# Optimization experiments

Measured on AMD Instinct MI355X. Metric: run time of the kernel, lower is better.

Reference implementation:

```python
import jax, jax.numpy as jnp
import numpy as np

R_CUT = 5.0
N_NODES = 50000
N_EDGES = 400000
N_GRAPHS = 2500
D = 128        # embedding_size (hardcoded by torch.split(..., 128))
N_RBF = 20
N_BLOCKS = 3
PI = 3.141592653589793


def setup_inputs() -> dict:
    key = jax.random.key(0)
    ks = jax.random.split(key, 32)
    w = lambda k, s: (jax.random.normal(k, s) * 0.05).astype(jnp.float32)
    z = jax.random.randint(ks[0], (N_NODES,), 0, 100)
    edges = jax.random.randint(ks[1], (N_EDGES, 2), 0, N_NODES)
    r_ij = jax.random.uniform(ks[2], (N_EDGES, 1), minval=0.8, maxval=R_CUT, dtype=jnp.float32)
    d = jax.random.normal(ks[3], (N_EDGES, 3), dtype=jnp.float32)
    r_ij_normalized = d / jnp.linalg.norm(d, axis=1, keepdims=True)
    graph_idx = jax.random.randint(ks[4], (N_NODES,), 0, N_GRAPHS)
    return {
        "z": z, "edges": edges, "r_ij": r_ij,
        "r_ij_normalized": r_ij_normalized, "graph_idx": graph_idx,
        "emb": w(ks[5], (100, D)),
        # message blocks (stacked over N_BLOCKS)
        "msg_w1": w(ks[6], (N_BLOCKS, D, D)),   "msg_b1": w(ks[7], (N_BLOCKS, D)),
        "msg_w2": w(ks[8], (N_BLOCKS, D, 3 * D)), "msg_b2": w(ks[9], (N_BLOCKS, 3 * D)),
        "rbf_w": w(ks[10], (N_BLOCKS, N_RBF, 3 * D)), "rbf_b": w(ks[11], (N_BLOCKS, 3 * D)),
        # update blocks
        "upd_U": w(ks[12], (N_BLOCKS, D, D)), "upd_V": w(ks[13], (N_BLOCKS, D, D)),
        "upd_w1": w(ks[14], (N_BLOCKS, 2 * D, D)), "upd_b1": w(ks[15], (N_BLOCKS, D)),
        "upd_w2": w(ks[16], (N_BLOCKS, D, 3 * D)), "upd_b2": w(ks[17], (N_BLOCKS, 3 * D)),
        # readout
        "blue_w1": w(ks[18], (D, D)), "blue_b1": w(ks[19], (D,)),
        "blue_w2": w(ks[20], (D, 1)), "blue_b2": w(ks[21], (1,)),
    }


def _rbf(r, r_cut):
    n = jnp.arange(1, N_RBF + 1, dtype=r.dtype)  # [20]
    return jnp.sin(n * PI / r_cut * r) / r        # [E,20]


def _fcut(r, r_cut):
    return jnp.where(r <= r_cut, 0.5 * (jnp.cos(PI * r / r_cut) + 1.0), 0.0)


def painn_forward(z, edges, r_ij, r_ij_normalized, graph_idx, emb,
                  msg_w1, msg_b1, msg_w2, msg_b2, rbf_w, rbf_b,
                  upd_U, upd_V, upd_w1, upd_b1, upd_w2, upd_b2,
                  blue_w1, blue_b1, blue_w2, blue_b2):
    silu = jax.nn.silu
    src = edges[:, 1]  # gathered (neighbor j)
    dst = edges[:, 0]  # scattered (center i)
    s = emb[z]                                           # [N,128]
    v = jnp.zeros((s.shape[0], 3, D), dtype=r_ij.dtype)  # [N,3,128]
    rbf = _rbf(r_ij, R_CUT)                              # [E,20]
    f_c = _fcut(r_ij, R_CUT)                             # [E,1]
    for i in range(N_BLOCKS):
        # --- message block ---
        rbf_fcut = (rbf @ rbf_w[i] + rbf_b[i]) * f_c            # [E,384]
        s_pass = silu(s @ msg_w1[i] + msg_b1[i]) @ msg_w2[i] + msg_b2[i]  # [N,384]
        pass_out = rbf_fcut * s_pass[src]                        # [E,384]
        d_v, d_s, d_rep = jnp.split(pass_out, 3, axis=-1)        # each [E,128]
        delta_v = v[src] * d_v[:, None, :] + r_ij_normalized[:, :, None] * d_rep[:, None, :]
        s = s + jax.ops.segment_sum(d_s, dst, num_segments=N_NODES)
        v = v + jax.ops.segment_sum(delta_v, dst, num_segments=N_NODES)
        # --- update block ---
        U_v = jnp.einsum('nde,ef->ndf', v, upd_U[i])             # [N,3,128]
        V_v = jnp.einsum('nde,ef->ndf', v, upd_V[i])
        V_norm = jnp.linalg.norm(V_v, axis=1)                    # [N,128]
        sv = jnp.concatenate([V_norm, s], axis=1)                # [N,256]
        a = silu(sv @ upd_w1[i] + upd_b1[i]) @ upd_w2[i] + upd_b2[i]  # [N,384]
        avv, asv, ass = jnp.split(a, 3, axis=1)
        s = s + jnp.sum(U_v * V_v, axis=1) * asv + ass
        v = v + avv[:, None, :] * U_v
    blue = silu(s @ blue_w1 + blue_b1) @ blue_w2 + blue_b2       # [N,1]
    return jax.ops.segment_sum(blue, graph_idx, num_segments=N_GRAPHS)  # [G,1]


def reference(z, edges, r_ij, r_ij_normalized, graph_idx, emb,
              msg_w1, msg_b1, msg_w2, msg_b2, rbf_w, rbf_b,
              upd_U, upd_V, upd_w1, upd_b1, upd_w2, upd_b2,
              blue_w1, blue_b1, blue_w2, blue_b2):
    return painn_forward(z, edges, r_ij, r_ij_normalized, graph_idx, emb,
                         msg_w1, msg_b1, msg_w2, msg_b2, rbf_w, rbf_b,
                         upd_U, upd_V, upd_w1, upd_b1, upd_w2, upd_b2,
                         blue_w1, blue_b1, blue_w2, blue_b2)
```

## Files before the change

### kernel.cpp

```cpp
#include <hip/hip_runtime.h>
#include <hip/hip_bf16.h>
#include <math.h>

#define N_NODES 50000
#define N_EDGES 400000
#define N_GRAPHS 2500
#define D 128
#define D3 384
#define N_RBF 20
#define R_CUT 5.0f
#define PI_F 3.14159265358979f
#define NCH 98
#define GEB 16

typedef __attribute__((ext_vector_type(8))) short bf16x8;
typedef __attribute__((ext_vector_type(4))) float f32x4;

__device__ __forceinline__ float silu_f(float x) {
    return x / (1.0f + __expf(-x));
}
__device__ __forceinline__ short f2bf(float x) {
    union { float f; unsigned u; } v; v.f = x;
    unsigned r = (v.u + 0x7FFFu + ((v.u >> 16) & 1u)) >> 16;
    return (short)r;
}
__device__ __forceinline__ float bf2f(short x) {
    union { unsigned u; float f; } v; v.u = ((unsigned)(unsigned short)x) << 16;
    return v.f;
}

#define MAXJOBS 19
struct PackJobs {
    const float* W[MAXJOBS];
    short* P[MAXJOBS];
    int K[MAXJOBS];
    int N[MAXJOBS];
    int boff[MAXJOBS + 1];
    int njobs;
};
__global__ void k_packall(PackJobs jobs) {
    int b = blockIdx.x;
    int j = 0;
    while (j + 1 < jobs.njobs && b >= jobs.boff[j + 1]) ++j;
    int t = (b - jobs.boff[j]) * 256 + threadIdx.x;
    int K = jobs.K[j], N = jobs.N[j];
    int NKT = K / 32;
    int total = (N / 16) * NKT * 64;
    if (t >= total) return;
    const float* W = jobs.W[j];
    short* P = jobs.P[j];
    int lane = t & 63;
    int kt = (t >> 6) % NKT;
    int nt = (t >> 6) / NKT;
    int k0 = kt * 32 + (lane >> 4) * 8;
    int col = nt * 16 + (lane & 15);
    #pragma unroll
    for (int q = 0; q < 8; ++q)
        P[(size_t)t * 8 + q] = f2bf(W[(size_t)(k0 + q) * N + col]);
}

__global__ void k_packrbf(const float* __restrict__ rbf_w, const float* __restrict__ rbf_b,
                          short* __restrict__ P) {
    int t = blockIdx.x * 256 + threadIdx.x;
    if (t >= 3 * 1536) return;
    int i = t / 1536;
    int r = t - i * 1536;
    int lane = r & 63;
    int nt = r >> 6;
    int col = nt * 16 + (lane & 15);
    int k0 = (lane >> 4) * 8;
    const float* W = rbf_w + (size_t)i * N_RBF * D3;
    const float* B = rbf_b + (size_t)i * D3;
    short* out = P + (size_t)i * 12288 + (size_t)r * 8;
    #pragma unroll
    for (int q = 0; q < 8; ++q) {
        int k = k0 + q;
        float v = (k < N_RBF) ? W[(size_t)k * D3 + col] : ((k == N_RBF) ? B[col] : 0.0f);
        out[q] = f2bf(v);
    }
}

template<int K, int N, bool SILU, int AMODE>
__global__ __launch_bounds__(256) void k_gemm(const void* __restrict__ Aptr,
                                              const void* __restrict__ A2ptr,
                                              const short* __restrict__ Bp,
                                              const float* __restrict__ bias,
                                              short* __restrict__ Cbf, int M) {
    constexpr int NKT = K / 32, NNT = N / 16;
    int lane = threadIdx.x & 63, wv = threadIdx.x >> 6;
    int tile = blockIdx.x * 4 + wv;
    if (tile * 16 >= M) return;
    int arow = tile * 16 + (lane & 15);
    int kgrp = (lane >> 4) * 8;

    bf16x8 a[NKT];
    if (AMODE == 0) {
        const short* A = (const short*)Aptr + (size_t)arow * K + kgrp;
        #pragma unroll
        for (int kt = 0; kt < NKT; ++kt) a[kt] = *(const bf16x8*)(A + kt * 32);
    } else if (AMODE == 1) {
        const float* A = (const float*)Aptr + (size_t)arow * K + kgrp;
        #pragma unroll
        for (int kt = 0; kt < NKT; ++kt)
            #pragma unroll
            for (int j = 0; j < 8; ++j) a[kt][j] = f2bf(A[kt * 32 + j]);
    } else {
        const short* A1 = (const short*)Aptr + (size_t)arow * 128 + kgrp;
        const float* A2 = (const float*)A2ptr + (size_t)arow * 128 + kgrp;
        #pragma unroll
        for (int kt = 0; kt < 4 && kt < NKT; ++kt) a[kt] = *(const bf16x8*)(A1 + kt * 32);
        #pragma unroll
        for (int kt = 4; kt < NKT; ++kt)
            #pragma unroll
            for (int j = 0; j < 8; ++j) a[kt][j] = f2bf(A2[(kt - 4) * 32 + j]);
    }

    int crow0 = tile * 16 + (lane >> 4) * 4;
    int ccol = lane & 15;
    const bf16x8* Bv = (const bf16x8*)Bp;
    #pragma unroll
    for (int nt = 0; nt < NNT; ++nt) {
        f32x4 acc = {0.f, 0.f, 0.f, 0.f};
        #pragma unroll
        for (int kt = 0; kt < NKT; ++kt) {
            bf16x8 b = Bv[(nt * NKT + kt) * 64 + lane];
            acc = __builtin_amdgcn_mfma_f32_16x16x32_bf16(a[kt], b, acc, 0, 0, 0);
        }
        int col = nt * 16 + ccol;
        float bs = bias ? bias[col] : 0.0f;
        #pragma unroll
        for (int j = 0; j < 4; ++j) {
            float v = acc[j] + bs;
            if (SILU) v = silu_f(v);
            Cbf[(size_t)(crow0 + j) * N + col] = f2bf(v);
        }
    }
}

__global__ void k_embed(const int* __restrict__ z, const float* __restrict__ emb,
                        float* __restrict__ s) {
    int i = blockIdx.x * blockDim.x + threadIdx.x;
    if (i < N_NODES * D) {
        int n = i >> 7, c = i & 127;
        s[i] = emb[z[n] * D + c];
    }
}

__global__ void k_hist(const int* __restrict__ edges, int* __restrict__ cnt) {
    int e = blockIdx.x * 256 + threadIdx.x;
    if (e < N_EDGES) atomicAdd(&cnt[edges[2 * e]], 1);
}

__global__ void k_scan1(const int* __restrict__ cnt, int* __restrict__ csum) {
    int t = threadIdx.x;
    int g = blockIdx.x * 512 + t;
    int v = (g < N_NODES) ? cnt[g] : 0;
    #pragma unroll
    for (int off = 32; off > 0; off >>= 1) v += __shfl_down(v, off, 64);
    __shared__ int ws[8];
    if ((t & 63) == 0) ws[t >> 6] = v;
    __syncthreads();
    if (t == 0) {
        int sum = 0;
        #pragma unroll
        for (int i = 0; i < 8; ++i) sum += ws[i];
        csum[blockIdx.x] = sum;
    }
}

__global__ void k_scan2(const int* __restrict__ csum, int* __restrict__ cbase) {
    if (threadIdx.x == 0 && blockIdx.x == 0) {
        int s = 0;
        for (int i = 0; i < NCH; ++i) { cbase[i] = s; s += csum[i]; }
    }
}

__global__ void k_scan3(const int* __restrict__ cnt, const int* __restrict__ cbase,
                        int* __restrict__ rowptr) {
    __shared__ int buf[512];
    int t = threadIdx.x;
    int g = blockIdx.x * 512 + t;
    int orig = (g < N_NODES) ? cnt[g] : 0;
    buf[t] = orig;
    __syncthreads();
    for (int off = 1; off < 512; off <<= 1) {
        int v = (t >= off) ? buf[t - off] : 0;
        __syncthreads();
        buf[t] += v;
        __syncthreads();
    }
    if (g < N_NODES) rowptr[g] = cbase[blockIdx.x] + buf[t] - orig;
    if (g == 0 && blockIdx.x == 0) rowptr[N_NODES] = N_EDGES;
}

__global__ void k_scatter(const int* __restrict__ edges, const float* __restrict__ r_ij,
                          const float* __restrict__ rhat, const int* __restrict__ rowptr,
                          int* __restrict__ cursor, int* __restrict__ esrc,
                          short* __restrict__ erbf, float4* __restrict__ erhat) {
    int e = blockIdx.x * 256 + threadIdx.x;
    if (e >= N_EDGES) return;
    int dst = edges[2 * e], src = edges[2 * e + 1];
    int p = rowptr[dst] + atomicAdd(&cursor[dst], 1);
    esrc[p] = src;
    float r = r_ij[e];
    float fc = (r <= R_CUT) ? 0.5f * (cosf(PI_F * r / R_CUT) + 1.0f) : 0.0f;
    float inv_r = 1.0f / r;
    short rec[32];
    #pragma unroll
    for (int k = 0; k < N_RBF; ++k)
        rec[k] = f2bf(sinf((float)(k + 1) * (PI_F / R_CUT) * r) * inv_r * fc);
    rec[20] = f2bf(fc);
    #pragma unroll
    for (int k = 21; k < 32; ++k) rec[k] = 0;
    short* out = erbf + (size_t)p * 32;
    #pragma unroll
    for (int k = 0; k < 32; ++k) out[k] = rec[k];
    float4 rh;
    rh.x = rhat[3 * e]; rh.y = rhat[3 * e + 1]; rh.z = rhat[3 * e + 2]; rh.w = 0.f;
    erhat[p] = rh;
}

__global__ __launch_bounds__(128, 4) void k_edge3(
    const int* __restrict__ rowptr, const int* __restrict__ esrc,
    const short* __restrict__ erbf, const float4* __restrict__ erhat,
    const short* __restrict__ pRbf,
    const short* __restrict__ spass, const short* __restrict__ vold,
    float* __restrict__ s, short* __restrict__ vnew) {
    __shared__ short gate_lds[GEB][D3];
    int tid = threadIdx.x;
    int lane = tid & 63;
    int wv = tid >> 6;
    int c = tid;
    int ntb = wv * 12;
    for (int n = blockIdx.x; n < N_NODES; n += gridDim.x) {
        int p0 = rowptr[n], p1 = rowptr[n + 1];
        float sa = 0.f, va0 = 0.f, va1 = 0.f, va2 = 0.f;
        for (int pb = p0; pb < p1; pb += GEB) {
            int erow = pb + (lane & 15);
            if (erow >= p1) erow = p1 - 1;
            bf16x8 afrag = *(const bf16x8*)(erbf + (size_t)erow * 32 + (lane >> 4) * 8);
            int r0 = (lane >> 4) * 4;
            int fcol = lane & 15;
            #pragma unroll
            for (int t = 0; t < 12; ++t) {
                int nt = ntb + t;
                bf16x8 b = *(const bf16x8*)(pRbf + ((size_t)(nt * 64 + lane)) * 8);
                f32x4 acc = {0.f, 0.f, 0.f, 0.f};
                acc = __builtin_amdgcn_mfma_f32_16x16x32_bf16(afrag, b, acc, 0, 0, 0);
                int col = nt * 16 + fcol;
                #pragma unroll
                for (int j = 0; j < 4; ++j)
                    gate_lds[r0 + j][col] = f2bf(acc[j]);
            }
            __syncthreads();
            int pe = (pb + GEB < p1) ? pb + GEB : p1;
            for (int p = pb; p < pe; ++p) {
                int src = esrc[p];
                float4 rh = erhat[p];
                const short* g = gate_lds[p - pb];
                float a0 = bf2f(g[c]);
                float a1 = bf2f(g[128 + c]);
                float a2 = bf2f(g[256 + c]);
                const short* sp = spass + (size_t)src * D3;
                float dv = a0 * bf2f(sp[c]);
                float ds = a1 * bf2f(sp[128 + c]);
                float dr = a2 * bf2f(sp[256 + c]);
                sa += ds;
                const short* vs = vold + (size_t)src * D3;
                va0 += bf2f(vs[c]) * dv + rh.x * dr;
                va1 += bf2f(vs[128 + c]) * dv + rh.y * dr;
                va2 += bf2f(vs[256 + c]) * dv + rh.z * dr;
            }
            __syncthreads();
        }
        s[(size_t)n * D + c] += sa;
        size_t vb = (size_t)n * D3;
        vnew[vb + c]       = f2bf(bf2f(vold[vb + c]) + va0);
        vnew[vb + 128 + c] = f2bf(bf2f(vold[vb + 128 + c]) + va1);
        vnew[vb + 256 + c] = f2bf(bf2f(vold[vb + 256 + c]) + va2);
    }
}

__global__ void k_svbuild(const short* __restrict__ Vv, short* __restrict__ Vn) {
    int i = blockIdx.x * 256 + threadIdx.x;
    int n = i >> 7, c = i & 127;
    float acc = 0.f;
    #pragma unroll
    for (int d = 0; d < 3; ++d) {
        float v = bf2f(Vv[(size_t)(n * 3 + d) * D + c]);
        acc += v * v;
    }
    Vn[i] = f2bf(sqrtf(acc));
}

__global__ void k_apply(float* __restrict__ s, short* __restrict__ v,
                        const short* __restrict__ Uv, const short* __restrict__ Vv,
                        const short* __restrict__ a_bf) {
    int i = blockIdx.x * 256 + threadIdx.x;
    int n = i >> 7, c = i & 127;
    float avv = bf2f(a_bf[(size_t)n * D3 + c]);
    float asv = bf2f(a_bf[(size_t)n * D3 + 128 + c]);
    float ass = bf2f(a_bf[(size_t)n * D3 + 256 + c]);
    float scal = 0.f;
    float uvr[3];
    #pragma unroll
    for (int d = 0; d < 3; ++d) {
        float u = bf2f(Uv[(size_t)(n * 3 + d) * D + c]);
        float vv = bf2f(Vv[(size_t)(n * 3 + d) * D + c]);
        uvr[d] = u;
        scal += u * vv;
    }
    s[i] += scal * asv + ass;
    #pragma unroll
    for (int d = 0; d < 3; ++d) {
        size_t idx = (size_t)n * D3 + d * 128 + c;
        v[idx] = f2bf(bf2f(v[idx]) + avv * uvr[d]);
    }
}

__global__ void k_blue_dot(const short* __restrict__ h, const int* __restrict__ graph_idx,
                           const float* __restrict__ w2, const float* __restrict__ b2,
                           float* __restrict__ out) {
    __shared__ float red[4];
    int c = threadIdx.x & 127;
    int n = blockIdx.x * 2 + (threadIdx.x >> 7);
    float val = bf2f(h[(size_t)n * D + c]) * w2[c];
    #pragma unroll
    for (int off = 32; off > 0; off >>= 1) val += __shfl_down(val, off, 64);
    if ((threadIdx.x & 63) == 0) red[threadIdx.x >> 6] = val;
    __syncthreads();
    if (threadIdx.x == 0)   atomicAdd(&out[graph_idx[n]], red[0] + red[1] + b2[0]);
    if (threadIdx.x == 128) atomicAdd(&out[graph_idx[n]], red[2] + red[3] + b2[0]);
}

static inline int gemm_grid(int M) { return (M / 16 + 3) / 4; }

extern "C" void kernel_launch(void* const* d_in, const int* in_sizes, int n_in,
                              void* d_out, int out_size, void* d_ws, size_t ws_size,
                              hipStream_t stream) {
    const int*   z         = (const int*)d_in[0];
    const int*   edges     = (const int*)d_in[1];
    const float* r_ij      = (const float*)d_in[2];
    const float* rhat      = (const float*)d_in[3];
    const int*   graph_idx = (const int*)d_in[4];
    const float* emb       = (const float*)d_in[5];
    const float* msg_w1    = (const float*)d_in[6];
    const float* msg_b1    = (const float*)d_in[7];
    const float* msg_w2    = (const float*)d_in[8];
    const float* msg_b2    = (const float*)d_in[9];
    const float* rbf_w     = (const float*)d_in[10];
    const float* rbf_b     = (const float*)d_in[11];
    const float* upd_U     = (const float*)d_in[12];
    const float* upd_V     = (const float*)d_in[13];
    const float* upd_w1    = (const float*)d_in[14];
    const float* upd_b1    = (const float*)d_in[15];
    const float* upd_w2    = (const float*)d_in[16];
    const float* upd_b2    = (const float*)d_in[17];
    const float* blue_w1   = (const float*)d_in[18];
    const float* blue_b1   = (const float*)d_in[19];
    const float* blue_w2   = (const float*)d_in[20];
    const float* blue_b2   = (const float*)d_in[21];
    float* out = (float*)d_out;

    char* ws = (char*)d_ws;
    size_t off = 0;
    auto alloc = [&](size_t bytes) { void* p = ws + off; off += (bytes + 255) & ~(size_t)255; return p; };

    float* s      = (float*)alloc((size_t)N_NODES * D * 4);
    short* bufV0  = (short*)alloc((size_t)N_NODES * D3 * 2);
    short* bufV1  = (short*)alloc((size_t)N_NODES * D3 * 2);
    short* shrd   = (short*)alloc((size_t)N_NODES * D3 * 2);
    short* hbuf   = (short*)alloc((size_t)N_NODES * D * 2);
    short* Vv     = (short*)alloc((size_t)N_NODES * D3 * 2);
    short* Vn     = shrd;
    int*    esrc   = (int*)alloc((size_t)N_EDGES * 4);
    short*  erbf   = (short*)alloc((size_t)N_EDGES * 32 * 2);
    float4* erhat  = (float4*)alloc((size_t)N_EDGES * 16);
    int*    rowptr = (int*)alloc((size_t)(N_NODES + 1) * 4);
    int*    cnt    = (int*)alloc((size_t)N_NODES * 4);
    int*    csum   = (int*)alloc(NCH * 4);
    int*    cbase  = (int*)alloc(NCH * 4);

    short* pBlue = (short*)alloc(16384 * 2);
    short* pRbfAll = (short*)alloc((size_t)3 * 12288 * 2);
    short* pMsgW1[3]; short* pMsgW2[3]; short* pU[3]; short* pV[3]; short* pUpdW1[3]; short* pUpdW2[3];
    for (int i = 0; i < 3; ++i) {
        pMsgW1[i] = (short*)alloc(16384 * 2);
        pMsgW2[i] = (short*)alloc(49152 * 2);
        pU[i]     = (short*)alloc(16384 * 2);
        pV[i]     = (short*)alloc(16384 * 2);
        pUpdW1[i] = (short*)alloc(32768 * 2);
        pUpdW2[i] = (short*)alloc(49152 * 2);
    }

    PackJobs jobs;
    jobs.njobs = 0;
    int bacc = 0;
    auto addjob = [&](const float* W, short* P, int K, int N) {
        int j = jobs.njobs++;
        jobs.W[j] = W; jobs.P[j] = P; jobs.K[j] = K; jobs.N[j] = N;
        jobs.boff[j] = bacc;
        int total = (N / 16) * (K / 32) * 64;
        bacc += (total + 255) / 256;
        jobs.boff[j + 1] = bacc;
    };
    addjob(blue_w1, pBlue, 128, 128);
    for (int i = 0; i < 3; ++i) {
        addjob(msg_w1 + (size_t)i * D * D,     pMsgW1[i], 128, 128);
        addjob(msg_w2 + (size_t)i * D * D3,    pMsgW2[i], 128, 384);
        addjob(upd_U  + (size_t)i * D * D,     pU[i],     128, 128);
        addjob(upd_V  + (size_t)i * D * D,     pV[i],     128, 128);
        addjob(upd_w1 + (size_t)i * 2 * D * D, pUpdW1[i], 256, 128);
        addjob(upd_w2 + (size_t)i * D * D3,    pUpdW2[i], 128, 384);
    }
    k_packall<<<bacc, 256, 0, stream>>>(jobs);
    k_packrbf<<<18, 256, 0, stream>>>(rbf_w, rbf_b, pRbfAll);

    hipMemsetAsync(cnt, 0, (size_t)N_NODES * 4, stream);
    k_hist<<<(N_EDGES + 255) / 256, 256, 0, stream>>>(edges, cnt);
    k_scan1<<<NCH, 512, 0, stream>>>(cnt, csum);
    k_scan2<<<1, 64, 0, stream>>>(csum, cbase);
    k_scan3<<<NCH, 512, 0, stream>>>(cnt, cbase, rowptr);
    hipMemsetAsync(cnt, 0, (size_t)N_NODES * 4, stream);
    k_scatter<<<(N_EDGES + 255) / 256, 256, 0, stream>>>(edges, r_ij, rhat, rowptr, cnt,
                                                         esrc, erbf, erhat);

    hipMemsetAsync(bufV0, 0, (size_t)N_NODES * D3 * 2, stream);
    hipMemsetAsync(d_out, 0, (size_t)out_size * sizeof(float), stream);
    k_embed<<<(N_NODES * D) / 256, 256, 0, stream>>>(z, emb, s);

    const int gN  = gemm_grid(N_NODES);
    const int gN3 = gemm_grid(N_NODES * 3);

    for (int i = 0; i < 3; ++i) {
        short* vstate = (i & 1) ? bufV1 : bufV0;
        short* vscr   = (i & 1) ? bufV0 : bufV1;
        k_gemm<128, 128, true, 1><<<gN, 256, 0, stream>>>(
            s, nullptr, pMsgW1[i], msg_b1 + (size_t)i * D, hbuf, N_NODES);
        k_gemm<128, 384, false, 0><<<gN, 256, 0, stream>>>(
            hbuf, nullptr, pMsgW2[i], msg_b2 + (size_t)i * D3, shrd, N_NODES);
        k_edge3<<<2048, 128, 0, stream>>>(rowptr, esrc, erbf, erhat,
                                          pRbfAll + (size_t)i * 12288,
                                          shrd, vstate, s, vscr);
        k_gemm<128, 128, false, 0><<<gN3, 256, 0, stream>>>(
            vscr, nullptr, pU[i], nullptr, vstate, N_NODES * 3);
        k_gemm<128, 128, false, 0><<<gN3, 256, 0, stream>>>(
            vscr, nullptr, pV[i], nullptr, Vv, N_NODES * 3);
        k_svbuild<<<(N_NODES * D) / 256, 256, 0, stream>>>(Vv, Vn);
        k_gemm<256, 128, true, 2><<<gN, 256, 0, stream>>>(
            Vn, s, pUpdW1[i], upd_b1 + (size_t)i * D, hbuf, N_NODES);
        k_gemm<128, 384, false, 0><<<gN, 256, 0, stream>>>(
            hbuf, nullptr, pUpdW2[i], upd_b2 + (size_t)i * D3, shrd, N_NODES);
        k_apply<<<(N_NODES * D) / 256, 256, 0, stream>>>(s, vscr, vstate, Vv, shrd);
    }

    k_gemm<128, 128, true, 1><<<gN, 256, 0, stream>>>(
        s, nullptr, pBlue, blue_b1, hbuf, N_NODES);
    k_blue_dot<<<N_NODES / 2, 256, 0, stream>>>(hbuf, graph_idx, blue_w2, blue_b2, out);
}
```

Measured before the change: 1.131 ms.

## Fuse U/V gemms and restructure edge kernel LDS usage and grid

Merges the two per-block U and V projections into one kernel that reads the vector state once and writes both outputs, with the packed weights placed contiguously. In the edge kernel, the RBF weight fragments are hoisted into registers outside the node loop. Edge source indices and unit vectors are staged in shared memory, the gate buffer gets a padded stride to reduce bank conflicts, and the grid is doubled. This cuts repeated global loads and one full pass over the vector state, at the cost of more registers per thread in both kernels.

```diff
diff --git a/kernel.cpp b/kernel.cpp
--- a/kernel.cpp
+++ b/kernel.cpp
@@ -12,6 +12,7 @@
 #define PI_F 3.14159265358979f
 #define NCH 98
 #define GEB 16
+#define GLDS_STRIDE 388
 
 typedef __attribute__((ext_vector_type(8))) short bf16x8;
 typedef __attribute__((ext_vector_type(4))) float f32x4;
@@ -137,6 +138,37 @@
     }
 }
 
+__global__ __launch_bounds__(256) void k_gemmUV(const short* __restrict__ A,
+                                                const short* __restrict__ Bp,
+                                                short* __restrict__ Cu,
+                                                short* __restrict__ Cv, int M) {
+    int lane = threadIdx.x & 63, wv = threadIdx.x >> 6;
+    int tile = blockIdx.x * 4 + wv;
+    if (tile * 16 >= M) return;
+    int arow = tile * 16 + (lane & 15);
+    int kgrp = (lane >> 4) * 8;
+    const short* Ar = A + (size_t)arow * 128 + kgrp;
+    bf16x8 a[4];
+    #pragma unroll
+    for (int kt = 0; kt < 4; ++kt) a[kt] = *(const bf16x8*)(Ar + kt * 32);
+    int crow0 = tile * 16 + (lane >> 4) * 4;
+    int ccol = lane & 15;
+    const bf16x8* Bv = (const bf16x8*)Bp;
+    #pragma unroll
+    for (int nt = 0; nt < 16; ++nt) {
+        f32x4 acc = {0.f, 0.f, 0.f, 0.f};
+        #pragma unroll
+        for (int kt = 0; kt < 4; ++kt)
+            acc = __builtin_amdgcn_mfma_f32_16x16x32_bf16(a[kt], Bv[(nt * 4 + kt) * 64 + lane], acc, 0, 0, 0);
+        int col = nt * 16 + ccol;
+        short* C = (col < 128) ? Cu : Cv;
+        int cc = col & 127;
+        #pragma unroll
+        for (int j = 0; j < 4; ++j)
+            C[(size_t)(crow0 + j) * 128 + cc] = f2bf(acc[j]);
+    }
+}
+
 __global__ void k_embed(const int* __restrict__ z, const float* __restrict__ emb,
                         float* __restrict__ s) {
     int i = blockIdx.x * blockDim.x + threadIdx.x;
@@ -226,12 +258,20 @@
     const short* __restrict__ pRbf,
     const short* __restrict__ spass, const short* __restrict__ vold,
     float* __restrict__ s, short* __restrict__ vnew) {
-    __shared__ short gate_lds[GEB][D3];
+    __shared__ short gate_lds[GEB * GLDS_STRIDE];
+    __shared__ int   src_lds[GEB];
+    __shared__ float4 rh_lds[GEB];
     int tid = threadIdx.x;
     int lane = tid & 63;
     int wv = tid >> 6;
     int c = tid;
     int ntb = wv * 12;
+    bf16x8 bfr[12];
+    #pragma unroll
+    for (int t = 0; t < 12; ++t)
+        bfr[t] = *(const bf16x8*)(pRbf + ((size_t)((ntb + t) * 64 + lane)) * 8);
+    int r0 = (lane >> 4) * 4;
+    int fcol = lane & 15;
     for (int n = blockIdx.x; n < N_NODES; n += gridDim.x) {
         int p0 = rowptr[n], p1 = rowptr[n + 1];
         float sa = 0.f, va0 = 0.f, va1 = 0.f, va2 = 0.f;
@@ -239,25 +279,25 @@
             int erow = pb + (lane & 15);
             if (erow >= p1) erow = p1 - 1;
             bf16x8 afrag = *(const bf16x8*)(erbf + (size_t)erow * 32 + (lane >> 4) * 8);
-            int r0 = (lane >> 4) * 4;
-            int fcol = lane & 15;
+            if (tid < GEB) {
+                int p = pb + tid;
+                if (p < p1) { src_lds[tid] = esrc[p]; rh_lds[tid] = erhat[p]; }
+            }
             #pragma unroll
             for (int t = 0; t < 12; ++t) {
-                int nt = ntb + t;
-                bf16x8 b = *(const bf16x8*)(pRbf + ((size_t)(nt * 64 + lane)) * 8);
                 f32x4 acc = {0.f, 0.f, 0.f, 0.f};
-                acc = __builtin_amdgcn_mfma_f32_16x16x32_bf16(afrag, b, acc, 0, 0, 0);
-                int col = nt * 16 + fcol;
+                acc = __builtin_amdgcn_mfma_f32_16x16x32_bf16(afrag, bfr[t], acc, 0, 0, 0);
+                int col = (ntb + t) * 16 + fcol;
                 #pragma unroll
                 for (int j = 0; j < 4; ++j)
-                    gate_lds[r0 + j][col] = f2bf(acc[j]);
+                    gate_lds[(r0 + j) * GLDS_STRIDE + col] = f2bf(acc[j]);
             }
             __syncthreads();
             int pe = (pb + GEB < p1) ? pb + GEB : p1;
             for (int p = pb; p < pe; ++p) {
-                int src = esrc[p];
-                float4 rh = erhat[p];
-                const short* g = gate_lds[p - pb];
+                int src = src_lds[p - pb];
+                float4 rh = rh_lds[p - pb];
+                const short* g = gate_lds + (p - pb) * GLDS_STRIDE;
                 float a0 = bf2f(g[c]);
                 float a1 = bf2f(g[128 + c]);
                 float a2 = bf2f(g[256 + c]);
@@ -383,12 +423,11 @@
 
     short* pBlue = (short*)alloc(16384 * 2);
     short* pRbfAll = (short*)alloc((size_t)3 * 12288 * 2);
-    short* pMsgW1[3]; short* pMsgW2[3]; short* pU[3]; short* pV[3]; short* pUpdW1[3]; short* pUpdW2[3];
+    short* pMsgW1[3]; short* pMsgW2[3]; short* pUV[3]; short* pUpdW1[3]; short* pUpdW2[3];
     for (int i = 0; i < 3; ++i) {
         pMsgW1[i] = (short*)alloc(16384 * 2);
         pMsgW2[i] = (short*)alloc(49152 * 2);
-        pU[i]     = (short*)alloc(16384 * 2);
-        pV[i]     = (short*)alloc(16384 * 2);
+        pUV[i]    = (short*)alloc(32768 * 2);
         pUpdW1[i] = (short*)alloc(32768 * 2);
         pUpdW2[i] = (short*)alloc(49152 * 2);
     }
@@ -408,8 +447,8 @@
     for (int i = 0; i < 3; ++i) {
         addjob(msg_w1 + (size_t)i * D * D,     pMsgW1[i], 128, 128);
         addjob(msg_w2 + (size_t)i * D * D3,    pMsgW2[i], 128, 384);
-        addjob(upd_U  + (size_t)i * D * D,     pU[i],     128, 128);
-        addjob(upd_V  + (size_t)i * D * D,     pV[i],     128, 128);
+        addjob(upd_U  + (size_t)i * D * D,     pUV[i],          128, 128);
+        addjob(upd_V  + (size_t)i * D * D,     pUV[i] + 16384,  128, 128);
         addjob(upd_w1 + (size_t)i * 2 * D * D, pUpdW1[i], 256, 128);
         addjob(upd_w2 + (size_t)i * D * D3,    pUpdW2[i], 128, 384);
     }
@@ -439,13 +478,10 @@
             s, nullptr, pMsgW1[i], msg_b1 + (size_t)i * D, hbuf, N_NODES);
         k_gemm<128, 384, false, 0><<<gN, 256, 0, stream>>>(
             hbuf, nullptr, pMsgW2[i], msg_b2 + (size_t)i * D3, shrd, N_NODES);
-        k_edge3<<<2048, 128, 0, stream>>>(rowptr, esrc, erbf, erhat,
+        k_edge3<<<4096, 128, 0, stream>>>(rowptr, esrc, erbf, erhat,
                                           pRbfAll + (size_t)i * 12288,
                                           shrd, vstate, s, vscr);
-        k_gemm<128, 128, false, 0><<<gN3, 256, 0, stream>>>(
-            vscr, nullptr, pU[i], nullptr, vstate, N_NODES * 3);
-        k_gemm<128, 128, false, 0><<<gN3, 256, 0, stream>>>(
-            vscr, nullptr, pV[i], nullptr, Vv, N_NODES * 3);
+        k_gemmUV<<<gN3, 256, 0, stream>>>(vscr, pUV[i], vstate, Vv, N_NODES * 3);
         k_svbuild<<<(N_NODES * D) / 256, 256, 0, stream>>>(Vv, Vn);
         k_gemm<256, 128, true, 2><<<gN, 256, 0, stream>>>(
             Vn, s, pUpdW1[i], upd_b1 + (size_t)i * D, hbuf, N_NODES);
```

Result: faster. 1.021 ms (-9.7%).
